# Performance work log

Hardware: AMD Instinct MI355X
Metric: run time of the kernel (lower is better)

The kernel has to match this reference:

```python
import jax, jax.numpy as jnp
import numpy as np

EPS = 1.0
POS_WEIGHT = 1.0
REDUCTION = 'mean'

N, D = 8192, 128
NUM_CLASSES = 32


def setup_inputs() -> dict:
    key = jax.random.key(0)
    k1, k2 = jax.random.split(key)
    ys = jax.random.normal(k1, (N, D), dtype=jnp.float32)
    labels = jax.random.randint(k2, (N,), 0, NUM_CLASSES, dtype=jnp.int64)
    return {"ys": ys, "labels": labels}


def reference(ys, labels):
    n = ys.shape[0]
    # Pairwise squared distances via one GEMM: ||a||^2 + ||b||^2 - 2 a.b
    sq = jnp.sum(ys * ys, axis=-1)                      # [N]
    d2 = sq[:, None] + sq[None, :] - 2.0 * (ys @ ys.T)  # [N, N]
    d2 = jnp.maximum(d2, 0.0)
    pair = jnp.triu(jnp.ones((n, n), dtype=bool), k=1)  # i < j, each unordered pair once
    same = labels[:, None] == labels[None, :]
    # positive-pair term: pos_weight * squared distance
    pos = POS_WEIGHT * d2
    # negative-pair term: clip(eps - sqrt(d2), 0)^2 ; guard sqrt(0) for unused entries
    neg_mask = pair & (~same)
    d = jnp.sqrt(jnp.where(neg_mask, d2, 1.0))
    neg = jnp.clip(EPS - d, 0.0) ** 2
    terms = jnp.where(same, pos, neg) * pair.astype(ys.dtype)
    loss = jnp.sum(terms)
    if REDUCTION == 'mean':
        loss = loss / (n * (n - 1) / 2)
    return loss.reshape(1)
```

## Files before the change

### kernel.cpp

```cpp
#include <hip/hip_runtime.h>
#include <stdint.h>
#include <math.h>

#define NN 8192
#define DD 128
#define NB 64
#define NBLK (NB * (NB + 1) / 2)
#define NC 32
#define NPB 256
#define RPB 32
#define TOTBLK (NBLK + NC)
#define SCALE (2.0f / ((float)NN * (float)(NN - 1)))

typedef __attribute__((ext_vector_type(4))) float f32x4;


__device__ __forceinline__ uint32_t pk4_fp8(float f0, float f1, float f2, float f3) {
    int d = __builtin_amdgcn_cvt_pk_fp8_f32(f0, f1, 0, false);
    d = __builtin_amdgcn_cvt_pk_fp8_f32(f2, f3, d, true);
    return (uint32_t)d;
}

__global__ __launch_bounds__(256) void prep_kernel(const float* __restrict__ ys,
                                                   const int* __restrict__ lab,
                                                   uint32_t* __restrict__ a8,
                                                   uint32_t* __restrict__ b8,
                                                   float* __restrict__ sq,
                                                   float* __restrict__ clspart,
                                                   float* __restrict__ out) {
    int b = blockIdx.x, t = threadIdx.x;
    __shared__ float cls[4][NC][DD];
    __shared__ int slab[RPB];

#pragma unroll
    for (int i = 0; i < 16; ++i) ((float4*)cls)[i * 256 + t] = make_float4(0.f, 0.f, 0.f, 0.f);
    if (t < RPB) slab[t] = lab[b * RPB + t];

#pragma unroll
    for (int u = 0; u < 2; ++u) {
        int rloc = (t >> 4) + u * 16;
        int c8 = t & 15;
        int row = b * RPB + rloc;
        const float* base = ys + (size_t)row * DD + c8 * 8;
        float4 v0 = *(const float4*)base;
        float4 v1 = *(const float4*)(base + 4);
        uint2 outB = make_uint2(pk4_fp8(v0.x, v0.y, v0.z, v0.w),
                                pk4_fp8(v1.x, v1.y, v1.z, v1.w));
        uint2 outA = make_uint2(pk4_fp8(-2.f * v0.x, -2.f * v0.y, -2.f * v0.z, -2.f * v0.w),
                                pk4_fp8(-2.f * v1.x, -2.f * v1.y, -2.f * v1.z, -2.f * v1.w));
        size_t off = (size_t)(b * 2 + u) * 2048 + (c8 >> 2) * 512 + (c8 & 3) * 128 + (rloc & 15) * 8;
        *(uint2*)((char*)b8 + off) = outB;
        *(uint2*)((char*)a8 + off) = outA;
        float s = v0.x * v0.x + v0.y * v0.y + v0.z * v0.z + v0.w * v0.w
                + v1.x * v1.x + v1.y * v1.y + v1.z * v1.z + v1.w * v1.w;
        s += __shfl_xor(s, 1); s += __shfl_xor(s, 2);
        s += __shfl_xor(s, 4); s += __shfl_xor(s, 8);
        if (c8 == 0) sq[row] = s;
    }
    __syncthreads();

    {
        int g = t >> 6, col0 = (t & 63) * 2;
#pragma unroll
        for (int rr = 0; rr < 8; ++rr) {
            int rloc = g * 8 + rr;
            float2 v = *(const float2*)(ys + (size_t)(b * RPB + rloc) * DD + col0);
            int lb = slab[rloc];
            cls[g][lb][col0]     += v.x;
            cls[g][lb][col0 + 1] += v.y;
        }
    }
    __syncthreads();
#pragma unroll
    for (int i = 0; i < 4; ++i) {
        int idx = i * 256 + t;
        float4 s0 = ((const float4*)cls[0])[idx];
        float4 s1 = ((const float4*)cls[1])[idx];
        float4 s2 = ((const float4*)cls[2])[idx];
        float4 s3 = ((const float4*)cls[3])[idx];
        ((float4*)(clspart + (size_t)b * NC * DD))[idx] =
            make_float4((s0.x + s1.x) + (s2.x + s3.x), (s0.y + s1.y) + (s2.y + s3.y),
                        (s0.z + s1.z) + (s2.z + s3.z), (s0.w + s1.w) + (s2.w + s3.w));
    }
    if (b == 0 && t == 0) out[0] = 0.f;
}

__global__ __launch_bounds__(256) void loss_kernel(const uint32_t* __restrict__ a8,
                                                   const uint32_t* __restrict__ b8,
                                                   const float* __restrict__ sq,
                                                   const int* __restrict__ lab,
                                                   const float* __restrict__ clspart,
                                                   const float* __restrict__ ys,
                                                   float* __restrict__ out) {
    int p = blockIdx.x, t = threadIdx.x;

    if (p < NC) {
        __shared__ float sp[2][DD];
        __shared__ float redc[4], reds[4], red2[2];
        int col = t & 127, half = t >> 7;
        float S0 = 0.f, S1 = 0.f, S2 = 0.f, S3 = 0.f;
        const float* cp = clspart + (size_t)half * 128 * NC * DD + p * DD + col;
#pragma unroll 8
        for (int pb = 0; pb < 128; pb += 4) {
            S0 += cp[(size_t)(pb + 0) * NC * DD];
            S1 += cp[(size_t)(pb + 1) * NC * DD];
            S2 += cp[(size_t)(pb + 2) * NC * DD];
            S3 += cp[(size_t)(pb + 3) * NC * DD];
        }
        sp[half][col] = (S0 + S1) + (S2 + S3);

        float cnt = 0.f, ssq = 0.f;
        for (int rr = t; rr < NN; rr += 256) {
            if (lab[rr] == p) { cnt += 1.f; ssq += sq[rr]; }
        }
#pragma unroll
        for (int off = 32; off >= 1; off >>= 1) {
            cnt += __shfl_down(cnt, off);
            ssq += __shfl_down(ssq, off);
        }
        if ((t & 63) == 0) { redc[t >> 6] = cnt; reds[t >> 6] = ssq; }
        __syncthreads();

        float s2 = 0.f;
        if (t < DD) { float Sc = sp[0][t] + sp[1][t]; s2 = Sc * Sc; }
#pragma unroll
        for (int off = 32; off >= 1; off >>= 1) s2 += __shfl_down(s2, off);
        if (t < 128 && (t & 63) == 0) red2[t >> 6] = s2;
        __syncthreads();
        if (t == 0) {
            float c = redc[0] + redc[1] + redc[2] + redc[3];
            float s = reds[0] + reds[1] + reds[2] + reds[3];
            atomicAdd(out, (c * s - (red2[0] + red2[1])) * SCALE);
        }
        return;
    }

    int pt = p - NC;
    int q = (NBLK - 1) - pt;
    int r = (int)((sqrtf(8.0f * (float)q + 1.0f) - 1.0f) * 0.5f);
    while (r * (r + 1) / 2 > q) --r;
    while ((r + 1) * (r + 2) / 2 <= q) ++r;
    int bi = (NB - 1) - r;
    int bj = (NB - 1) - (q - r * (r + 1) / 2);
    int i0 = bi * 128, j0 = bj * 128;

    int wave = t >> 6, lane = t & 63;
    int wm = wave >> 1, wn = wave & 1;
    int lr = lane & 15, lg = lane >> 4;

    f32x4 acc[4][4];
#pragma unroll
    for (int m = 0; m < 4; ++m)
#pragma unroll
        for (int n = 0; n < 4; ++n) acc[m][n] = (f32x4){0.f, 0.f, 0.f, 0.f};

    const char* pa = (const char*)a8 + ((size_t)(i0 >> 4) + wm * 4) * 2048 + lg * 128 + lr * 8;
    const char* pbp = (const char*)b8 + ((size_t)(j0 >> 4) + wn * 4) * 2048 + lg * 128 + lr * 8;

#pragma unroll
    for (int ks = 0; ks < 4; ++ks) {
        long af[4], bf[4];
#pragma unroll
        for (int m = 0; m < 4; ++m) af[m] = *(const long*)(pa + m * 2048 + ks * 512);
#pragma unroll
        for (int n = 0; n < 4; ++n) bf[n] = *(const long*)(pbp + n * 2048 + ks * 512);
#pragma unroll
        for (int m = 0; m < 4; ++m)
#pragma unroll
            for (int n = 0; n < 4; ++n)
                acc[m][n] = __builtin_amdgcn_mfma_f32_16x16x32_fp8_fp8(af[m], bf[n], acc[m][n], 0, 0, 0);
    }

    float msi = fminf(sq[i0 + lane * 2], sq[i0 + lane * 2 + 1]);
    float msj = fminf(sq[j0 + lane * 2], sq[j0 + lane * 2 + 1]);
#pragma unroll
    for (int off = 32; off >= 1; off >>= 1) {
        msi = fminf(msi, __shfl_xor(msi, off));
        msj = fminf(msj, __shfl_xor(msj, off));
    }
    float mn = acc[0][0][0];
#pragma unroll
    for (int m = 0; m < 4; ++m)
#pragma unroll
        for (int n = 0; n < 4; ++n)
#pragma unroll
            for (int qq = 0; qq < 4; ++qq) mn = fminf(mn, acc[m][n][qq]);

    if (__any(mn + msi + msj < 20.0f)) {
        float ns = 0.f;
#pragma unroll
        for (int m = 0; m < 4; ++m)
#pragma unroll
            for (int n = 0; n < 4; ++n)
#pragma unroll
                for (int qq = 0; qq < 4; ++qq) {
                    int i = i0 + wm * 64 + m * 16 + lg * 4 + qq;
                    int j = j0 + wn * 64 + n * 16 + lr;
                    float d2a = acc[m][n][qq] + sq[i] + sq[j];
                    if (d2a < 20.0f && i < j && lab[i] != lab[j]) {
                        float d2e = 0.f;
                        for (int d = 0; d < DD; ++d) {
                            float df = ys[(size_t)i * DD + d] - ys[(size_t)j * DD + d];
                            d2e += df * df;
                        }
                        if (d2e < 1.0f) { float e = 1.0f - sqrtf(d2e); ns += e * e; }
                    }
                }
        if (ns != 0.f) atomicAdd(out, ns * SCALE);
    }
}

extern "C" void kernel_launch(void* const* d_in, const int* in_sizes, int n_in,
                              void* d_out, int out_size, void* d_ws, size_t ws_size,
                              hipStream_t stream) {
    const float* ys = (const float*)d_in[0];
    const int* lab = (const int*)d_in[1];
    float* out = (float*)d_out;

    char* w = (char*)d_ws;
    uint32_t* a8    = (uint32_t*)(w);
    uint32_t* b8    = (uint32_t*)(w + 1048576);
    float* sq       = (float*)(w + 2097152);
    float* clspart  = (float*)(w + 2129920);

    prep_kernel<<<NPB, 256, 0, stream>>>(ys, lab, a8, b8, sq, clspart, out);
    loss_kernel<<<TOTBLK, 256, 0, stream>>>(a8, b8, sq, lab, clspart, ys, out);
}
```

Baseline: 32.17 us.

## Switch pairwise GEMM to bf16 MFMA with LDS staging and block swizzle

Replaces the fp8 operand packing and fp8 MFMA with bf16 operands (with -2y made by exact bit manipulation) and bf16 16x16x32 MFMA. Tiles are staged through 64KB of shared memory using global_load_lds, and the block index is remapped across groups of 8. The aim is higher screening accuracy so fewer tiles take the exact fp32 fallback path, plus better memory locality. In exchange it doubles operand bytes and the per-block LDS footprint, which limits occupancy.

```diff
diff --git a/kernel.cpp b/kernel.cpp
--- a/kernel.cpp
+++ b/kernel.cpp
@@ -12,19 +12,20 @@
 #define TOTBLK (NBLK + NC)
 #define SCALE (2.0f / ((float)NN * (float)(NN - 1)))
 
+typedef __attribute__((ext_vector_type(8))) short short8;
 typedef __attribute__((ext_vector_type(4))) float f32x4;
 
-
-__device__ __forceinline__ uint32_t pk4_fp8(float f0, float f1, float f2, float f3) {
-    int d = __builtin_amdgcn_cvt_pk_fp8_f32(f0, f1, 0, false);
-    d = __builtin_amdgcn_cvt_pk_fp8_f32(f2, f3, d, true);
-    return (uint32_t)d;
-}
+__device__ __forceinline__ unsigned short f2bf_rne(float x) {
+    union { float f; uint32_t u; } v; v.f = x;
+    uint32_t r = v.u + 0x7FFFu + ((v.u >> 16) & 1u);
+    return (unsigned short)(r >> 16);
+}
+
 
 __global__ __launch_bounds__(256) void prep_kernel(const float* __restrict__ ys,
                                                    const int* __restrict__ lab,
-                                                   uint32_t* __restrict__ a8,
-                                                   uint32_t* __restrict__ b8,
+                                                   unsigned short* __restrict__ a2y,
+                                                   unsigned short* __restrict__ ybf,
                                                    float* __restrict__ sq,
                                                    float* __restrict__ clspart,
                                                    float* __restrict__ out) {
@@ -44,13 +45,18 @@
         const float* base = ys + (size_t)row * DD + c8 * 8;
         float4 v0 = *(const float4*)base;
         float4 v1 = *(const float4*)(base + 4);
-        uint2 outB = make_uint2(pk4_fp8(v0.x, v0.y, v0.z, v0.w),
-                                pk4_fp8(v1.x, v1.y, v1.z, v1.w));
-        uint2 outA = make_uint2(pk4_fp8(-2.f * v0.x, -2.f * v0.y, -2.f * v0.z, -2.f * v0.w),
-                                pk4_fp8(-2.f * v1.x, -2.f * v1.y, -2.f * v1.z, -2.f * v1.w));
-        size_t off = (size_t)(b * 2 + u) * 2048 + (c8 >> 2) * 512 + (c8 & 3) * 128 + (rloc & 15) * 8;
-        *(uint2*)((char*)b8 + off) = outB;
-        *(uint2*)((char*)a8 + off) = outA;
+        uint32_t w0 = (uint32_t)f2bf_rne(v0.x) | ((uint32_t)f2bf_rne(v0.y) << 16);
+        uint32_t w1 = (uint32_t)f2bf_rne(v0.z) | ((uint32_t)f2bf_rne(v0.w) << 16);
+        uint32_t w2 = (uint32_t)f2bf_rne(v1.x) | ((uint32_t)f2bf_rne(v1.y) << 16);
+        uint32_t w3 = (uint32_t)f2bf_rne(v1.z) | ((uint32_t)f2bf_rne(v1.w) << 16);
+        uint4 outB = make_uint4(w0, w1, w2, w3);
+        uint4 outA = make_uint4((w0 + 0x00800080u) ^ 0x80008000u,
+                                (w1 + 0x00800080u) ^ 0x80008000u,
+                                (w2 + 0x00800080u) ^ 0x80008000u,
+                                (w3 + 0x00800080u) ^ 0x80008000u);
+        size_t off = (size_t)(b * 2 + u) * 4096 + c8 * 256 + (rloc & 15) * 16;
+        *(uint4*)((char*)ybf + off) = outB;
+        *(uint4*)((char*)a2y + off) = outA;
         float s = v0.x * v0.x + v0.y * v0.y + v0.z * v0.z + v0.w * v0.w
                 + v1.x * v1.x + v1.y * v1.y + v1.z * v1.z + v1.w * v1.w;
         s += __shfl_xor(s, 1); s += __shfl_xor(s, 2);
@@ -85,18 +91,22 @@
     if (b == 0 && t == 0) out[0] = 0.f;
 }
 
-__global__ __launch_bounds__(256) void loss_kernel(const uint32_t* __restrict__ a8,
-                                                   const uint32_t* __restrict__ b8,
-                                                   const float* __restrict__ sq,
-                                                   const int* __restrict__ lab,
-                                                   const float* __restrict__ clspart,
-                                                   const float* __restrict__ ys,
-                                                   float* __restrict__ out) {
-    int p = blockIdx.x, t = threadIdx.x;
+__global__ __launch_bounds__(256, 2) void loss_kernel(const unsigned short* __restrict__ a2y,
+                                                      const unsigned short* __restrict__ ybf,
+                                                      const float* __restrict__ sq,
+                                                      const int* __restrict__ lab,
+                                                      const float* __restrict__ clspart,
+                                                      const float* __restrict__ ys,
+                                                      float* __restrict__ out) {
+    __shared__ __align__(16) unsigned char sm[65536];
+    int b = blockIdx.x, t = threadIdx.x;
+    int p = (b & 7) * 264 + (b >> 3);
 
     if (p < NC) {
-        __shared__ float sp[2][DD];
-        __shared__ float redc[4], reds[4], red2[2];
+        float* sp   = (float*)sm;
+        float* redc = (float*)(sm + 1024);
+        float* reds = (float*)(sm + 1088);
+        float* red2 = (float*)(sm + 1152);
         int col = t & 127, half = t >> 7;
         float S0 = 0.f, S1 = 0.f, S2 = 0.f, S3 = 0.f;
         const float* cp = clspart + (size_t)half * 128 * NC * DD + p * DD + col;
@@ -107,7 +117,7 @@
             S2 += cp[(size_t)(pb + 2) * NC * DD];
             S3 += cp[(size_t)(pb + 3) * NC * DD];
         }
-        sp[half][col] = (S0 + S1) + (S2 + S3);
+        sp[half * 128 + col] = (S0 + S1) + (S2 + S3);
 
         float cnt = 0.f, ssq = 0.f;
         for (int rr = t; rr < NN; rr += 256) {
@@ -122,7 +132,7 @@
         __syncthreads();
 
         float s2 = 0.f;
-        if (t < DD) { float Sc = sp[0][t] + sp[1][t]; s2 = Sc * Sc; }
+        if (t < DD) { float Sc = sp[t] + sp[128 + t]; s2 = Sc * Sc; }
 #pragma unroll
         for (int off = 32; off >= 1; off >>= 1) s2 += __shfl_down(s2, off);
         if (t < 128 && (t & 63) == 0) red2[t >> 6] = s2;
@@ -148,27 +158,43 @@
     int wm = wave >> 1, wn = wave & 1;
     int lr = lane & 15, lg = lane >> 4;
 
+    {
+        const char* gsrc = (wave < 2)
+            ? ((const char*)a2y + (size_t)(i0 >> 4) * 4096 + wave * 16384)
+            : ((const char*)ybf + (size_t)(j0 >> 4) * 4096 + (wave - 2) * 16384);
+        unsigned lbase = wave * 16384;
+#pragma unroll
+        for (int it = 0; it < 16; ++it) {
+            __builtin_amdgcn_global_load_lds(
+                (const uint32_t*)(gsrc + it * 1024 + lane * 16),
+                (uint32_t*)(sm + lbase + it * 1024), 16, 0, 0);
+        }
+    }
+    asm volatile("s_waitcnt vmcnt(0)");
+    __syncthreads();
+
     f32x4 acc[4][4];
 #pragma unroll
     for (int m = 0; m < 4; ++m)
 #pragma unroll
         for (int n = 0; n < 4; ++n) acc[m][n] = (f32x4){0.f, 0.f, 0.f, 0.f};
 
-    const char* pa = (const char*)a8 + ((size_t)(i0 >> 4) + wm * 4) * 2048 + lg * 128 + lr * 8;
-    const char* pbp = (const char*)b8 + ((size_t)(j0 >> 4) + wn * 4) * 2048 + lg * 128 + lr * 8;
+    const unsigned char* pA = sm + wm * 16384;
+    const unsigned char* pB = sm + 32768 + wn * 16384;
+    int foff = lg * 256 + lr * 16;
 
 #pragma unroll
     for (int ks = 0; ks < 4; ++ks) {
-        long af[4], bf[4];
-#pragma unroll
-        for (int m = 0; m < 4; ++m) af[m] = *(const long*)(pa + m * 2048 + ks * 512);
-#pragma unroll
-        for (int n = 0; n < 4; ++n) bf[n] = *(const long*)(pbp + n * 2048 + ks * 512);
+        short8 af[4], bf[4];
+#pragma unroll
+        for (int m = 0; m < 4; ++m) af[m] = *(const short8*)(pA + m * 4096 + ks * 1024 + foff);
+#pragma unroll
+        for (int n = 0; n < 4; ++n) bf[n] = *(const short8*)(pB + n * 4096 + ks * 1024 + foff);
 #pragma unroll
         for (int m = 0; m < 4; ++m)
 #pragma unroll
             for (int n = 0; n < 4; ++n)
-                acc[m][n] = __builtin_amdgcn_mfma_f32_16x16x32_fp8_fp8(af[m], bf[n], acc[m][n], 0, 0, 0);
+                acc[m][n] = __builtin_amdgcn_mfma_f32_16x16x32_bf16(af[m], bf[n], acc[m][n], 0, 0, 0);
     }
 
     float msi = fminf(sq[i0 + lane * 2], sq[i0 + lane * 2 + 1]);
@@ -218,11 +244,11 @@
     float* out = (float*)d_out;
 
     char* w = (char*)d_ws;
-    uint32_t* a8    = (uint32_t*)(w);
-    uint32_t* b8    = (uint32_t*)(w + 1048576);
-    float* sq       = (float*)(w + 2097152);
-    float* clspart  = (float*)(w + 2129920);
-
-    prep_kernel<<<NPB, 256, 0, stream>>>(ys, lab, a8, b8, sq, clspart, out);
-    loss_kernel<<<TOTBLK, 256, 0, stream>>>(a8, b8, sq, lab, clspart, ys, out);
-}
+    unsigned short* a2y = (unsigned short*)(w);
+    unsigned short* ybf = (unsigned short*)(w + 2097152);
+    float* sq       = (float*)(w + 4194304);
+    float* clspart  = (float*)(w + 4227072);
+
+    prep_kernel<<<NPB, 256, 0, stream>>>(ys, lab, a2y, ybf, sq, clspart, out);
+    loss_kernel<<<TOTBLK, 256, 0, stream>>>(a2y, ybf, sq, lab, clspart, ys, out);
+}
```

New measurement: 35.98 us. 1.12x slower.

## Split class reduction into separate kernel, process two tiles per block

Applied to the files above, without the earlier changes.

Moves the per-class sum/count reduction out of the loss kernel into its own 160-block kernel that reduces partial class sums with a shared-memory tree. The pairwise loss kernel now handles two triangular tiles per block, halving its grid. Per-tile row minimum of squared norms is precomputed in the prep kernel, so the early-exit test no longer needs a wave shuffle reduction over sq. It also hoists the i<j check ahead of the sq loads. Adds a third kernel launch and longer-running blocks, with fewer blocks to balance load.

```diff
diff --git a/kernel.cpp b/kernel.cpp
--- a/kernel.cpp
+++ b/kernel.cpp
@@ -9,7 +9,7 @@
 #define NC 32
 #define NPB 256
 #define RPB 32
-#define TOTBLK (NBLK + NC)
+#define NTB (NBLK / 2)
 #define SCALE (2.0f / ((float)NN * (float)(NN - 1)))
 
 typedef __attribute__((ext_vector_type(4))) float f32x4;
@@ -27,15 +27,19 @@
                                                    uint32_t* __restrict__ b8,
                                                    float* __restrict__ sq,
                                                    float* __restrict__ clspart,
+                                                   float* __restrict__ tminpart,
                                                    float* __restrict__ out) {
     int b = blockIdx.x, t = threadIdx.x;
     __shared__ float cls[4][NC][DD];
     __shared__ int slab[RPB];
+    __shared__ int tmn;
 
 #pragma unroll
     for (int i = 0; i < 16; ++i) ((float4*)cls)[i * 256 + t] = make_float4(0.f, 0.f, 0.f, 0.f);
     if (t < RPB) slab[t] = lab[b * RPB + t];
-
+    if (t == 0) tmn = 0x7f800000;
+
+    float myMin = 1e30f;
 #pragma unroll
     for (int u = 0; u < 2; ++u) {
         int rloc = (t >> 4) + u * 16;
@@ -55,9 +59,11 @@
                 + v1.x * v1.x + v1.y * v1.y + v1.z * v1.z + v1.w * v1.w;
         s += __shfl_xor(s, 1); s += __shfl_xor(s, 2);
         s += __shfl_xor(s, 4); s += __shfl_xor(s, 8);
-        if (c8 == 0) sq[row] = s;
-    }
+        if (c8 == 0) { sq[row] = s; myMin = fminf(myMin, s); }
+    }
+    if ((t & 15) == 0) atomicMin(&tmn, __float_as_int(myMin));
     __syncthreads();
+    if (t == 0) tminpart[b] = __int_as_float(tmn);
 
     {
         int g = t >> 6, col0 = (t & 63) * 2;
@@ -85,129 +91,158 @@
     if (b == 0 && t == 0) out[0] = 0.f;
 }
 
+__global__ __launch_bounds__(256) void classred_kernel(const float* __restrict__ clspart,
+                                                       const int* __restrict__ lab,
+                                                       const float* __restrict__ sq,
+                                                       float* __restrict__ out) {
+    int g = blockIdx.x, t = threadIdx.x;
+    __shared__ float4 red[8][256];
+
+    if (g < 128) {
+        int c = g >> 2, q = g & 3;
+        const float4* base = (const float4*)(clspart + (size_t)t * NC * DD + c * DD + q * 32);
+        float4 v[8];
+#pragma unroll
+        for (int j = 0; j < 8; ++j) v[j] = base[j];
+#pragma unroll
+        for (int j = 0; j < 8; ++j) red[j][t] = v[j];
+        __syncthreads();
+#pragma unroll
+        for (int s = 128; s >= 1; s >>= 1) {
+            if (t < s) {
+#pragma unroll
+                for (int j = 0; j < 8; ++j) {
+                    float4 a = red[j][t], b2 = red[j][t + s];
+                    red[j][t] = make_float4(a.x + b2.x, a.y + b2.y, a.z + b2.z, a.w + b2.w);
+                }
+            }
+            __syncthreads();
+        }
+        if (t == 0) {
+            float s2 = 0.f;
+#pragma unroll
+            for (int j = 0; j < 8; ++j) {
+                float4 a = red[j][0];
+                s2 += a.x * a.x + a.y * a.y + a.z * a.z + a.w * a.w;
+            }
+            atomicAdd(out, -s2 * SCALE);
+        }
+    } else {
+        int c = g - 128;
+        float cnt = 0.f, ssq = 0.f;
+#pragma unroll 4
+        for (int rr = t; rr < NN; rr += 256) {
+            int lb = lab[rr]; float s = sq[rr];
+            if (lb == c) { cnt += 1.f; ssq += s; }
+        }
+#pragma unroll
+        for (int off = 32; off >= 1; off >>= 1) {
+            cnt += __shfl_down(cnt, off);
+            ssq += __shfl_down(ssq, off);
+        }
+        __shared__ float rc[4], rs[4];
+        if ((t & 63) == 0) { rc[t >> 6] = cnt; rs[t >> 6] = ssq; }
+        __syncthreads();
+        if (t == 0) {
+            float C = (rc[0] + rc[1]) + (rc[2] + rc[3]);
+            float S = (rs[0] + rs[1]) + (rs[2] + rs[3]);
+            atomicAdd(out, C * S * SCALE);
+        }
+    }
+}
+
 __global__ __launch_bounds__(256) void loss_kernel(const uint32_t* __restrict__ a8,
                                                    const uint32_t* __restrict__ b8,
                                                    const float* __restrict__ sq,
                                                    const int* __restrict__ lab,
-                                                   const float* __restrict__ clspart,
+                                                   const float* __restrict__ tminpart,
                                                    const float* __restrict__ ys,
                                                    float* __restrict__ out) {
     int p = blockIdx.x, t = threadIdx.x;
 
-    if (p < NC) {
-        __shared__ float sp[2][DD];
-        __shared__ float redc[4], reds[4], red2[2];
-        int col = t & 127, half = t >> 7;
-        float S0 = 0.f, S1 = 0.f, S2 = 0.f, S3 = 0.f;
-        const float* cp = clspart + (size_t)half * 128 * NC * DD + p * DD + col;
-#pragma unroll 8
-        for (int pb = 0; pb < 128; pb += 4) {
-            S0 += cp[(size_t)(pb + 0) * NC * DD];
-            S1 += cp[(size_t)(pb + 1) * NC * DD];
-            S2 += cp[(size_t)(pb + 2) * NC * DD];
-            S3 += cp[(size_t)(pb + 3) * NC * DD];
-        }
-        sp[half][col] = (S0 + S1) + (S2 + S3);
-
-        float cnt = 0.f, ssq = 0.f;
-        for (int rr = t; rr < NN; rr += 256) {
-            if (lab[rr] == p) { cnt += 1.f; ssq += sq[rr]; }
-        }
-#pragma unroll
-        for (int off = 32; off >= 1; off >>= 1) {
-            cnt += __shfl_down(cnt, off);
-            ssq += __shfl_down(ssq, off);
-        }
-        if ((t & 63) == 0) { redc[t >> 6] = cnt; reds[t >> 6] = ssq; }
-        __syncthreads();
-
-        float s2 = 0.f;
-        if (t < DD) { float Sc = sp[0][t] + sp[1][t]; s2 = Sc * Sc; }
-#pragma unroll
-        for (int off = 32; off >= 1; off >>= 1) s2 += __shfl_down(s2, off);
-        if (t < 128 && (t & 63) == 0) red2[t >> 6] = s2;
-        __syncthreads();
-        if (t == 0) {
-            float c = redc[0] + redc[1] + redc[2] + redc[3];
-            float s = reds[0] + reds[1] + reds[2] + reds[3];
-            atomicAdd(out, (c * s - (red2[0] + red2[1])) * SCALE);
-        }
-        return;
-    }
-
-    int pt = p - NC;
-    int q = (NBLK - 1) - pt;
+    int pt0 = p * 2;
+    int q = (NBLK - 1) - pt0;
     int r = (int)((sqrtf(8.0f * (float)q + 1.0f) - 1.0f) * 0.5f);
     while (r * (r + 1) / 2 > q) --r;
     while ((r + 1) * (r + 2) / 2 <= q) ++r;
     int bi = (NB - 1) - r;
     int bj = (NB - 1) - (q - r * (r + 1) / 2);
-    int i0 = bi * 128, j0 = bj * 128;
 
     int wave = t >> 6, lane = t & 63;
     int wm = wave >> 1, wn = wave & 1;
     int lr = lane & 15, lg = lane >> 4;
-
-    f32x4 acc[4][4];
-#pragma unroll
-    for (int m = 0; m < 4; ++m)
-#pragma unroll
-        for (int n = 0; n < 4; ++n) acc[m][n] = (f32x4){0.f, 0.f, 0.f, 0.f};
-
-    const char* pa = (const char*)a8 + ((size_t)(i0 >> 4) + wm * 4) * 2048 + lg * 128 + lr * 8;
-    const char* pbp = (const char*)b8 + ((size_t)(j0 >> 4) + wn * 4) * 2048 + lg * 128 + lr * 8;
-
-#pragma unroll
-    for (int ks = 0; ks < 4; ++ks) {
-        long af[4], bf[4];
-#pragma unroll
-        for (int m = 0; m < 4; ++m) af[m] = *(const long*)(pa + m * 2048 + ks * 512);
-#pragma unroll
-        for (int n = 0; n < 4; ++n) bf[n] = *(const long*)(pbp + n * 2048 + ks * 512);
+    int lo = lg * 128 + lr * 8;
+
+    float total_ns = 0.f;
+
+#pragma unroll 1
+    for (int tt = 0; tt < 2; ++tt) {
+        int i0 = bi * 128, j0 = bj * 128;
+
+        float4 ti = ((const float4*)tminpart)[bi];
+        float4 tj = ((const float4*)tminpart)[bj];
+        float tb = fminf(fminf(ti.x, ti.y), fminf(ti.z, ti.w))
+                 + fminf(fminf(tj.x, tj.y), fminf(tj.z, tj.w));
+
+        const char* pa = (const char*)a8 + ((size_t)bi * 8 + wm * 4) * 2048 + lo;
+        const char* pbp = (const char*)b8 + ((size_t)bj * 8 + wn * 4) * 2048 + lo;
+
+        f32x4 acc[4][4];
 #pragma unroll
         for (int m = 0; m < 4; ++m)
 #pragma unroll
+            for (int n = 0; n < 4; ++n) acc[m][n] = (f32x4){0.f, 0.f, 0.f, 0.f};
+
+#pragma unroll
+        for (int ks = 0; ks < 4; ++ks) {
+            long af[4], bf[4];
+#pragma unroll
+            for (int m = 0; m < 4; ++m) af[m] = *(const long*)(pa + m * 2048 + ks * 512);
+#pragma unroll
+            for (int n = 0; n < 4; ++n) bf[n] = *(const long*)(pbp + n * 2048 + ks * 512);
+#pragma unroll
+            for (int m = 0; m < 4; ++m)
+#pragma unroll
+                for (int n = 0; n < 4; ++n)
+                    acc[m][n] = __builtin_amdgcn_mfma_f32_16x16x32_fp8_fp8(af[m], bf[n], acc[m][n], 0, 0, 0);
+        }
+
+        float mn = acc[0][0][0];
+#pragma unroll
+        for (int m = 0; m < 4; ++m)
+#pragma unroll
             for (int n = 0; n < 4; ++n)
-                acc[m][n] = __builtin_amdgcn_mfma_f32_16x16x32_fp8_fp8(af[m], bf[n], acc[m][n], 0, 0, 0);
-    }
-
-    float msi = fminf(sq[i0 + lane * 2], sq[i0 + lane * 2 + 1]);
-    float msj = fminf(sq[j0 + lane * 2], sq[j0 + lane * 2 + 1]);
-#pragma unroll
-    for (int off = 32; off >= 1; off >>= 1) {
-        msi = fminf(msi, __shfl_xor(msi, off));
-        msj = fminf(msj, __shfl_xor(msj, off));
-    }
-    float mn = acc[0][0][0];
-#pragma unroll
-    for (int m = 0; m < 4; ++m)
-#pragma unroll
-        for (int n = 0; n < 4; ++n)
-#pragma unroll
-            for (int qq = 0; qq < 4; ++qq) mn = fminf(mn, acc[m][n][qq]);
-
-    if (__any(mn + msi + msj < 20.0f)) {
-        float ns = 0.f;
-#pragma unroll
-        for (int m = 0; m < 4; ++m)
-#pragma unroll
-            for (int n = 0; n < 4; ++n)
-#pragma unroll
-                for (int qq = 0; qq < 4; ++qq) {
-                    int i = i0 + wm * 64 + m * 16 + lg * 4 + qq;
-                    int j = j0 + wn * 64 + n * 16 + lr;
-                    float d2a = acc[m][n][qq] + sq[i] + sq[j];
-                    if (d2a < 20.0f && i < j && lab[i] != lab[j]) {
-                        float d2e = 0.f;
-                        for (int d = 0; d < DD; ++d) {
-                            float df = ys[(size_t)i * DD + d] - ys[(size_t)j * DD + d];
-                            d2e += df * df;
+#pragma unroll
+                for (int qq = 0; qq < 4; ++qq) mn = fminf(mn, acc[m][n][qq]);
+
+        if (__any(mn + tb < 20.0f)) {
+#pragma unroll
+            for (int m = 0; m < 4; ++m)
+#pragma unroll
+                for (int n = 0; n < 4; ++n)
+#pragma unroll
+                    for (int qq = 0; qq < 4; ++qq) {
+                        int i = i0 + wm * 64 + m * 16 + lg * 4 + qq;
+                        int j = j0 + wn * 64 + n * 16 + lr;
+                        if (i < j) {
+                            float d2a = acc[m][n][qq] + sq[i] + sq[j];
+                            if (d2a < 20.0f && lab[i] != lab[j]) {
+                                float d2e = 0.f;
+                                for (int d = 0; d < DD; ++d) {
+                                    float df = ys[(size_t)i * DD + d] - ys[(size_t)j * DD + d];
+                                    d2e += df * df;
+                                }
+                                if (d2e < 1.0f) { float e = 1.0f - sqrtf(d2e); total_ns += e * e; }
+                            }
                         }
-                        if (d2e < 1.0f) { float e = 1.0f - sqrtf(d2e); ns += e * e; }
                     }
-                }
-        if (ns != 0.f) atomicAdd(out, ns * SCALE);
-    }
+        }
+
+        ++bj;
+        if (bj == NB) { ++bi; bj = bi; }
+    }
+
+    if (total_ns != 0.f) atomicAdd(out, total_ns * SCALE);
 }
 
 extern "C" void kernel_launch(void* const* d_in, const int* in_sizes, int n_in,
@@ -218,11 +253,13 @@
     float* out = (float*)d_out;
 
     char* w = (char*)d_ws;
-    uint32_t* a8    = (uint32_t*)(w);
-    uint32_t* b8    = (uint32_t*)(w + 1048576);
-    float* sq       = (float*)(w + 2097152);
-    float* clspart  = (float*)(w + 2129920);
-
-    prep_kernel<<<NPB, 256, 0, stream>>>(ys, lab, a8, b8, sq, clspart, out);
-    loss_kernel<<<TOTBLK, 256, 0, stream>>>(a8, b8, sq, lab, clspart, ys, out);
-}
+    uint32_t* a8     = (uint32_t*)(w);
+    uint32_t* b8     = (uint32_t*)(w + 1048576);
+    float* sq        = (float*)(w + 2097152);
+    float* clspart   = (float*)(w + 2129920);
+    float* tminpart  = (float*)(w + 6324224);
+
+    prep_kernel<<<NPB, 256, 0, stream>>>(ys, lab, a8, b8, sq, clspart, tminpart, out);
+    classred_kernel<<<160, 256, 0, stream>>>(clspart, lab, sq, out);
+    loss_kernel<<<NTB, 256, 0, stream>>>(a8, b8, sq, lab, tminpart, ys, out);
+}
```

After: 40.92 us. 27.2% more time.

## Use 256x256 pair tiles with 512-thread blocks and precomputed row-norm minima

Applied to the files above, without the earlier changes.

Doubles the pair tile size to 256x256 with 8 waves per block, giving each wave 8x4 MFMA accumulators. This cuts the number of tile blocks and the per-block overhead of index decode, launch and the early-out check. The prep kernel now also stores each 32-row block's minimum squared norm, so the loss kernel builds its skip bound from eight cached values instead of reloading sq and doing shuffle reductions. The trade-offs are higher register pressure from 128 accumulator floats, fewer blocks for load balancing, and wasted work on the diagonal tiles.

```diff
diff --git a/kernel.cpp b/kernel.cpp
--- a/kernel.cpp
+++ b/kernel.cpp
@@ -4,12 +4,13 @@
 
 #define NN 8192
 #define DD 128
-#define NB 64
-#define NBLK (NB * (NB + 1) / 2)
+#define BT 256
+#define NB2 (NN / BT)
+#define NBLK2 (NB2 * (NB2 + 1) / 2)
 #define NC 32
 #define NPB 256
 #define RPB 32
-#define TOTBLK (NBLK + NC)
+#define TOT2 (NBLK2 + NC)
 #define SCALE (2.0f / ((float)NN * (float)(NN - 1)))
 
 typedef __attribute__((ext_vector_type(4))) float f32x4;
@@ -27,15 +28,19 @@
                                                    uint32_t* __restrict__ b8,
                                                    float* __restrict__ sq,
                                                    float* __restrict__ clspart,
+                                                   float* __restrict__ tminpart,
                                                    float* __restrict__ out) {
     int b = blockIdx.x, t = threadIdx.x;
     __shared__ float cls[4][NC][DD];
     __shared__ int slab[RPB];
+    __shared__ int tmn;
 
 #pragma unroll
     for (int i = 0; i < 16; ++i) ((float4*)cls)[i * 256 + t] = make_float4(0.f, 0.f, 0.f, 0.f);
     if (t < RPB) slab[t] = lab[b * RPB + t];
-
+    if (t == 0) tmn = 0x7f800000;
+
+    float myMin = 1e30f;
 #pragma unroll
     for (int u = 0; u < 2; ++u) {
         int rloc = (t >> 4) + u * 16;
@@ -55,9 +60,11 @@
                 + v1.x * v1.x + v1.y * v1.y + v1.z * v1.z + v1.w * v1.w;
         s += __shfl_xor(s, 1); s += __shfl_xor(s, 2);
         s += __shfl_xor(s, 4); s += __shfl_xor(s, 8);
-        if (c8 == 0) sq[row] = s;
-    }
+        if (c8 == 0) { sq[row] = s; myMin = fminf(myMin, s); }
+    }
+    if ((t & 15) == 0) atomicMin(&tmn, __float_as_int(myMin));
     __syncthreads();
+    if (t == 0) tminpart[b] = __int_as_float(tmn);
 
     {
         int g = t >> 6, col0 = (t & 63) * 2;
@@ -85,32 +92,34 @@
     if (b == 0 && t == 0) out[0] = 0.f;
 }
 
-__global__ __launch_bounds__(256) void loss_kernel(const uint32_t* __restrict__ a8,
-                                                   const uint32_t* __restrict__ b8,
-                                                   const float* __restrict__ sq,
-                                                   const int* __restrict__ lab,
-                                                   const float* __restrict__ clspart,
-                                                   const float* __restrict__ ys,
-                                                   float* __restrict__ out) {
+__global__ __launch_bounds__(512, 2) void loss_kernel(const uint32_t* __restrict__ a8,
+                                                      const uint32_t* __restrict__ b8,
+                                                      const float* __restrict__ sq,
+                                                      const int* __restrict__ lab,
+                                                      const float* __restrict__ clspart,
+                                                      const float* __restrict__ tminpart,
+                                                      const float* __restrict__ ys,
+                                                      float* __restrict__ out) {
     int p = blockIdx.x, t = threadIdx.x;
 
     if (p < NC) {
-        __shared__ float sp[2][DD];
-        __shared__ float redc[4], reds[4], red2[2];
-        int col = t & 127, half = t >> 7;
+        __shared__ float sp[4][DD];
+        __shared__ float rc[8], rs[8], red2[2];
+        int col = t & 127, grp = t >> 7;
+        const float* cp = clspart + (size_t)(grp * 64) * NC * DD + p * DD + col;
         float S0 = 0.f, S1 = 0.f, S2 = 0.f, S3 = 0.f;
-        const float* cp = clspart + (size_t)half * 128 * NC * DD + p * DD + col;
-#pragma unroll 8
-        for (int pb = 0; pb < 128; pb += 4) {
+#pragma unroll 4
+        for (int pb = 0; pb < 64; pb += 4) {
             S0 += cp[(size_t)(pb + 0) * NC * DD];
             S1 += cp[(size_t)(pb + 1) * NC * DD];
             S2 += cp[(size_t)(pb + 2) * NC * DD];
             S3 += cp[(size_t)(pb + 3) * NC * DD];
         }
-        sp[half][col] = (S0 + S1) + (S2 + S3);
+        sp[grp][col] = (S0 + S1) + (S2 + S3);
 
         float cnt = 0.f, ssq = 0.f;
-        for (int rr = t; rr < NN; rr += 256) {
+#pragma unroll 4
+        for (int rr = t; rr < NN; rr += 512) {
             if (lab[rr] == p) { cnt += 1.f; ssq += sq[rr]; }
         }
 #pragma unroll
@@ -118,92 +127,107 @@
             cnt += __shfl_down(cnt, off);
             ssq += __shfl_down(ssq, off);
         }
-        if ((t & 63) == 0) { redc[t >> 6] = cnt; reds[t >> 6] = ssq; }
+        if ((t & 63) == 0) { rc[t >> 6] = cnt; rs[t >> 6] = ssq; }
         __syncthreads();
 
         float s2 = 0.f;
-        if (t < DD) { float Sc = sp[0][t] + sp[1][t]; s2 = Sc * Sc; }
+        if (t < DD) {
+            float Sc = (sp[0][t] + sp[1][t]) + (sp[2][t] + sp[3][t]);
+            s2 = Sc * Sc;
+        }
 #pragma unroll
         for (int off = 32; off >= 1; off >>= 1) s2 += __shfl_down(s2, off);
         if (t < 128 && (t & 63) == 0) red2[t >> 6] = s2;
         __syncthreads();
         if (t == 0) {
-            float c = redc[0] + redc[1] + redc[2] + redc[3];
-            float s = reds[0] + reds[1] + reds[2] + reds[3];
-            atomicAdd(out, (c * s - (red2[0] + red2[1])) * SCALE);
+            float C = ((rc[0] + rc[1]) + (rc[2] + rc[3])) + ((rc[4] + rc[5]) + (rc[6] + rc[7]));
+            float S = ((rs[0] + rs[1]) + (rs[2] + rs[3])) + ((rs[4] + rs[5]) + (rs[6] + rs[7]));
+            atomicAdd(out, (C * S - (red2[0] + red2[1])) * SCALE);
         }
         return;
     }
 
     int pt = p - NC;
-    int q = (NBLK - 1) - pt;
+    int q = (NBLK2 - 1) - pt;
     int r = (int)((sqrtf(8.0f * (float)q + 1.0f) - 1.0f) * 0.5f);
     while (r * (r + 1) / 2 > q) --r;
     while ((r + 1) * (r + 2) / 2 <= q) ++r;
-    int bi = (NB - 1) - r;
-    int bj = (NB - 1) - (q - r * (r + 1) / 2);
-    int i0 = bi * 128, j0 = bj * 128;
+    int bi = (NB2 - 1) - r;
+    int bj = (NB2 - 1) - (q - r * (r + 1) / 2);
+    int i0 = bi * BT, j0 = bj * BT;
 
     int wave = t >> 6, lane = t & 63;
-    int wm = wave >> 1, wn = wave & 1;
+    int wm = wave >> 2, wn = wave & 3;
     int lr = lane & 15, lg = lane >> 4;
-
-    f32x4 acc[4][4];
-#pragma unroll
-    for (int m = 0; m < 4; ++m)
+    int lo = lg * 128 + lr * 8;
+
+    float tb;
+    {
+        const float4* tp = (const float4*)tminpart;
+        float4 a0 = tp[bi * 2], a1 = tp[bi * 2 + 1];
+        float4 c0 = tp[bj * 2], c1 = tp[bj * 2 + 1];
+        float mi = fminf(fminf(fminf(a0.x, a0.y), fminf(a0.z, a0.w)),
+                         fminf(fminf(a1.x, a1.y), fminf(a1.z, a1.w)));
+        float mj = fminf(fminf(fminf(c0.x, c0.y), fminf(c0.z, c0.w)),
+                         fminf(fminf(c1.x, c1.y), fminf(c1.z, c1.w)));
+        tb = mi + mj;
+    }
+
+    const char* pa = (const char*)a8 + ((size_t)bi * 16 + wm * 8) * 2048 + lo;
+    const char* pbp = (const char*)b8 + ((size_t)bj * 16 + wn * 4) * 2048 + lo;
+
+    f32x4 acc[8][4];
+#pragma unroll
+    for (int m = 0; m < 8; ++m)
 #pragma unroll
         for (int n = 0; n < 4; ++n) acc[m][n] = (f32x4){0.f, 0.f, 0.f, 0.f};
 
-    const char* pa = (const char*)a8 + ((size_t)(i0 >> 4) + wm * 4) * 2048 + lg * 128 + lr * 8;
-    const char* pbp = (const char*)b8 + ((size_t)(j0 >> 4) + wn * 4) * 2048 + lg * 128 + lr * 8;
-
 #pragma unroll
     for (int ks = 0; ks < 4; ++ks) {
-        long af[4], bf[4];
-#pragma unroll
-        for (int m = 0; m < 4; ++m) af[m] = *(const long*)(pa + m * 2048 + ks * 512);
+        long af[8], bf[4];
+#pragma unroll
+        for (int m = 0; m < 8; ++m) af[m] = *(const long*)(pa + m * 2048 + ks * 512);
 #pragma unroll
         for (int n = 0; n < 4; ++n) bf[n] = *(const long*)(pbp + n * 2048 + ks * 512);
 #pragma unroll
-        for (int m = 0; m < 4; ++m)
+        for (int m = 0; m < 8; ++m)
 #pragma unroll
             for (int n = 0; n < 4; ++n)
                 acc[m][n] = __builtin_amdgcn_mfma_f32_16x16x32_fp8_fp8(af[m], bf[n], acc[m][n], 0, 0, 0);
     }
 
-    float msi = fminf(sq[i0 + lane * 2], sq[i0 + lane * 2 + 1]);
-    float msj = fminf(sq[j0 + lane * 2], sq[j0 + lane * 2 + 1]);
-#pragma unroll
-    for (int off = 32; off >= 1; off >>= 1) {
-        msi = fminf(msi, __shfl_xor(msi, off));
-        msj = fminf(msj, __shfl_xor(msj, off));
-    }
-    float mn = acc[0][0][0];
-#pragma unroll
-    for (int m = 0; m < 4; ++m)
-#pragma unroll
-        for (int n = 0; n < 4; ++n)
-#pragma unroll
-            for (int qq = 0; qq < 4; ++qq) mn = fminf(mn, acc[m][n][qq]);
-
-    if (__any(mn + msi + msj < 20.0f)) {
+    float m0 = acc[0][0][0], m1 = acc[0][0][1], m2 = acc[0][0][2], m3 = acc[0][0][3];
+#pragma unroll
+    for (int m = 0; m < 8; ++m)
+#pragma unroll
+        for (int n = 0; n < 4; ++n) {
+            m0 = fminf(m0, acc[m][n][0]);
+            m1 = fminf(m1, acc[m][n][1]);
+            m2 = fminf(m2, acc[m][n][2]);
+            m3 = fminf(m3, acc[m][n][3]);
+        }
+    float mn = fminf(fminf(m0, m1), fminf(m2, m3));
+
+    if (__any(mn + tb < 20.0f)) {
         float ns = 0.f;
 #pragma unroll
-        for (int m = 0; m < 4; ++m)
+        for (int m = 0; m < 8; ++m)
 #pragma unroll
             for (int n = 0; n < 4; ++n)
 #pragma unroll
                 for (int qq = 0; qq < 4; ++qq) {
-                    int i = i0 + wm * 64 + m * 16 + lg * 4 + qq;
+                    int i = i0 + wm * 128 + m * 16 + lg * 4 + qq;
                     int j = j0 + wn * 64 + n * 16 + lr;
-                    float d2a = acc[m][n][qq] + sq[i] + sq[j];
-                    if (d2a < 20.0f && i < j && lab[i] != lab[j]) {
-                        float d2e = 0.f;
-                        for (int d = 0; d < DD; ++d) {
-                            float df = ys[(size_t)i * DD + d] - ys[(size_t)j * DD + d];
-                            d2e += df * df;
+                    if (i < j) {
+                        float d2a = acc[m][n][qq] + sq[i] + sq[j];
+                        if (d2a < 20.0f && lab[i] != lab[j]) {
+                            float d2e = 0.f;
+                            for (int d = 0; d < DD; ++d) {
+                                float df = ys[(size_t)i * DD + d] - ys[(size_t)j * DD + d];
+                                d2e += df * df;
+                            }
+                            if (d2e < 1.0f) { float e = 1.0f - sqrtf(d2e); ns += e * e; }
                         }
-                        if (d2e < 1.0f) { float e = 1.0f - sqrtf(d2e); ns += e * e; }
                     }
                 }
         if (ns != 0.f) atomicAdd(out, ns * SCALE);
@@ -218,11 +242,12 @@
     float* out = (float*)d_out;
 
     char* w = (char*)d_ws;
-    uint32_t* a8    = (uint32_t*)(w);
-    uint32_t* b8    = (uint32_t*)(w + 1048576);
-    float* sq       = (float*)(w + 2097152);
-    float* clspart  = (float*)(w + 2129920);
-
-    prep_kernel<<<NPB, 256, 0, stream>>>(ys, lab, a8, b8, sq, clspart, out);
-    loss_kernel<<<TOTBLK, 256, 0, stream>>>(a8, b8, sq, lab, clspart, ys, out);
-}
+    uint32_t* a8     = (uint32_t*)(w);
+    uint32_t* b8     = (uint32_t*)(w + 1048576);
+    float* sq        = (float*)(w + 2097152);
+    float* clspart   = (float*)(w + 2129920);
+    float* tminpart  = (float*)(w + 6324224);
+
+    prep_kernel<<<NPB, 256, 0, stream>>>(ys, lab, a8, b8, sq, clspart, tminpart, out);
+    loss_kernel<<<TOT2, 512, 0, stream>>>(a8, b8, sq, lab, clspart, tminpart, ys, out);
+}
```

New measurement: 36.83 us. +14.5%, slower.
